# Kernel tuning notes

Measured on AMD Instinct MI355X. Metric: run time of the kernel, lower is better.

Reference implementation:

```python
import jax, jax.numpy as jnp
import numpy as np

BS = 128
HW = 128
REG = 0.1


def setup_inputs() -> dict:
    key = jax.random.key(0)
    k1, k2 = jax.random.split(key)
    x1 = jax.random.normal(k1, (BS, 1, HW, HW), dtype=jnp.float32)
    x2 = jax.random.normal(k2, (BS, 1, HW, HW), dtype=jnp.float32)
    return {"x1": x1, "x2": x2}


def _calc_psd(x):
    # x: [2*bs, H, W]
    dft = jnp.fft.fft2(x)
    avgpsd = jnp.mean((dft * jnp.conj(dft)).real, axis=0)  # [H, W]
    return jnp.mean(jnp.log(avgpsd)) - jnp.log(jnp.mean(avgpsd))


def reference(x1, x2):
    a = x1[:, 0]  # [bs, H, W] (squeeze channel)
    b = x2[:, 0]
    # pairwise Frobenius distances: Dist[i, j] = ||x1[i] - x2[j]||_F
    diff = a[:, None, :, :] - b[None, :, :, :]          # [bs, bs, H, W]
    Dist = jnp.sqrt(jnp.sum(diff * diff, axis=(-2, -1)))  # [bs, bs]
    bs = Dist.shape[0]
    # CrossEntropyLoss(Dist, arange(bs)) = mean_i(logsumexp(Dist[i]) - Dist[i, i])
    log_probs = jax.nn.log_softmax(Dist, axis=-1)
    ce = -jnp.mean(jnp.diagonal(log_probs))
    # PSD regularizer on cat(x1, x2)
    x = jnp.concatenate([a, b], axis=0)  # [2*bs, H, W]
    r = _calc_psd(x)
    return ce - REG * r
```

## Files before the change

kernel.cpp:

```cpp
#include <hip/hip_runtime.h>
#include <math.h>


#define WS_N     0
#define WS_G     256
#define WS_NP    16640
#define WS_GP    20736
#define WS_P     4215040
#define WS_PS    6344960
#define WS_PL    6345025

#define PI_F 3.14159265358979323846f

__global__ __launch_bounds__(256) void ocl_gram(const float* __restrict__ A_,
                                                const float* __restrict__ B_,
                                                float* __restrict__ ws) {
    __shared__ float4 As[128 * 16];
    __shared__ float4 Bs[128 * 16];
    int ks = blockIdx.x;
    int k0q = ks * 16;
    int t = threadIdx.x;
    const float4* A = (const float4*)A_;
    const float4* B = (const float4*)B_;

    {
        int qi = t & 15, r0 = t >> 4;
        #pragma unroll
        for (int p = 0; p < 8; ++p) {
            int r = r0 + 16 * p;
            int sq = qi ^ ((r >> 3) & 7);
            As[r * 16 + sq] = A[(size_t)r * 4096 + k0q + qi];
            Bs[r * 16 + sq] = B[(size_t)r * 4096 + k0q + qi];
        }
    }
    __syncthreads();

    int ty = t >> 4, tx = t & 15;
    float acc[8][8];
    #pragma unroll
    for (int r = 0; r < 8; ++r)
        #pragma unroll
        for (int c = 0; c < 8; ++c) acc[r][c] = 0.0f;

    for (int qk = 0; qk < 16; ++qk) {
        int sa = qk ^ (ty & 7);
        int sb = qk ^ (tx & 7);
        float4 a4[8], b4[8];
        #pragma unroll
        for (int r = 0; r < 8; ++r) a4[r] = As[(ty * 8 + r) * 16 + sa];
        #pragma unroll
        for (int c = 0; c < 8; ++c) b4[c] = Bs[(tx * 8 + c) * 16 + sb];
        #pragma unroll
        for (int r = 0; r < 8; ++r)
            #pragma unroll
            for (int c = 0; c < 8; ++c) {
                float4 a = a4[r], b = b4[c];
                acc[r][c] = fmaf(a.x, b.x, fmaf(a.y, b.y,
                            fmaf(a.z, b.z, fmaf(a.w, b.w, acc[r][c]))));
            }
    }

    float4* Gq = (float4*)(ws + WS_GP + (size_t)ks * 16384);
    #pragma unroll
    for (int r = 0; r < 8; ++r)
        #pragma unroll
        for (int cc = 0; cc < 2; ++cc)
            Gq[(ty * 8 + r) * 32 + tx * 2 + cc] =
                make_float4(acc[r][cc * 4 + 0], acc[r][cc * 4 + 1],
                            acc[r][cc * 4 + 2], acc[r][cc * 4 + 3]);
}

__device__ __forceinline__ void fft128_reg(float& s0r, float& s0i,
                                           float& s1r, float& s1i,
                                           float cA, float sA,
                                           const float* wr, const float* wi,
                                           int lane) {
    float er = s0r + s1r, ei = s0i + s1i;
    float dr = s0r - s1r, di = s0i - s1i;
    float orr = dr * cA - di * sA;
    float oii = dr * sA + di * cA;
    #pragma unroll
    for (int st = 0; st < 6; ++st) {
        int m = 32 >> st;
        bool up = (lane & m) == 0;
        float tr = __shfl_xor(er, m), ti = __shfl_xor(ei, m);
        float ar = tr - er, ai = ti - ei;
        float e2r = up ? (er + tr) : (ar * wr[st] - ai * wi[st]);
        float e2i = up ? (ei + ti) : (ar * wi[st] + ai * wr[st]);
        tr = __shfl_xor(orr, m); ti = __shfl_xor(oii, m);
        float br_ = tr - orr, bi_ = ti - oii;
        float o2r = up ? (orr + tr) : (br_ * wr[st] - bi_ * wi[st]);
        float o2i = up ? (oii + ti) : (br_ * wi[st] + bi_ * wr[st]);
        er = e2r; ei = e2i; orr = o2r; oii = o2i;
    }
    s0r = er; s0i = ei; s1r = orr; s1i = oii;
}

__global__ __launch_bounds__(1024) void ocl_fft_psd(const float* __restrict__ x1,
                                                    const float* __restrict__ x2,
                                                    float* __restrict__ ws) {
    __shared__ float zre[64 * 128];
    __shared__ float zim[64 * 128];
    int t = threadIdx.x, lane = t & 63, wave = t >> 6;
    int img = blockIdx.x;
    float* P = ws + WS_P + (size_t)img * 8320;
    const float* src = (img < 128) ? (x1 + (size_t)img * 16384)
                                   : (x2 + (size_t)(img - 128) * 16384);

    float cA, sA, wr[6], wi[6];
    {
        float th = -PI_F * (float)lane / 64.0f;
        sA = __sinf(th); cA = __cosf(th);
        #pragma unroll
        for (int st = 0; st < 6; ++st) {
            int m = 32 >> st;
            float a = -PI_F * (float)(lane & (m - 1)) / (float)m;
            wi[st] = __sinf(a); wr[st] = __cosf(a);
        }
    }
    int rb = (int)(__brev((unsigned)lane) >> 26);

    float nrm = 0.0f;
    #pragma unroll
    for (int pi = 0; pi < 4; ++pi) {
        int p = wave * 4 + pi;
        const float* r0 = src + p * 256 + lane;
        float s0r = r0[0],   s1r = r0[64];
        float s0i = r0[128], s1i = r0[192];
        nrm += s0r * s0r + s1r * s1r + s0i * s0i + s1i * s1i;
        fft128_reg(s0r, s0i, s1r, s1i, cA, sA, wr, wi, lane);
        int f0 = (2 * rb + p) & 127;
        int f1 = (2 * rb + 1 + p) & 127;
        zre[p * 128 + f0] = s0r; zim[p * 128 + f0] = s0i;
        zre[p * 128 + f1] = s1r; zim[p * 128 + f1] = s1i;
    }
    for (int off = 32; off >= 1; off >>= 1) nrm += __shfl_xor(nrm, off);
    if (lane == 0) ws[WS_NP + img * 16 + wave] = nrm;
    __syncthreads();

    int p0 = (lane >> 1), p1 = 32 + (lane >> 1);
    int par = lane & 1;
    for (int k = wave; k < 65; k += 16) {
        float v0r, v0i, v1r, v1i;
        if (k == 0 || k == 64) {
            int c0 = (k + p0) & 127, c1 = (k + p1) & 127;
            float Z0r = zre[p0 * 128 + c0], Z0i = zim[p0 * 128 + c0];
            float Z1r = zre[p1 * 128 + c1], Z1i = zim[p1 * 128 + c1];
            v0r = par ? Z0i : Z0r; v0i = 0.0f;
            v1r = par ? Z1i : Z1r; v1i = 0.0f;
        } else {
            int kn = 128 - k;
            int ck = (k + p0) & 127, cn = (kn + p0) & 127;
            float Zkr = zre[p0 * 128 + ck], Zki = zim[p0 * 128 + ck];
            float Znr = zre[p0 * 128 + cn], Zni = zim[p0 * 128 + cn];
            float e0r = 0.5f * (Zkr + Znr), e0i = 0.5f * (Zki - Zni);
            float q0r = 0.5f * (Zki + Zni), q0i = 0.5f * (Znr - Zkr);
            v0r = par ? q0r : e0r; v0i = par ? q0i : e0i;
            ck = (k + p1) & 127; cn = (kn + p1) & 127;
            Zkr = zre[p1 * 128 + ck]; Zki = zim[p1 * 128 + ck];
            Znr = zre[p1 * 128 + cn]; Zni = zim[p1 * 128 + cn];
            float e1r = 0.5f * (Zkr + Znr), e1i = 0.5f * (Zki - Zni);
            float q1r = 0.5f * (Zki + Zni), q1i = 0.5f * (Znr - Zkr);
            v1r = par ? q1r : e1r; v1i = par ? q1i : e1i;
        }
        fft128_reg(v0r, v0i, v1r, v1i, cA, sA, wr, wi, lane);
        P[k * 128 + lane]      = v0r * v0r + v0i * v0i;
        P[k * 128 + 64 + lane] = v1r * v1r + v1i * v1i;
    }
}

__global__ __launch_bounds__(256) void ocl_reduce(float* __restrict__ ws) {
    int bid = blockIdx.x, t = threadIdx.x;
    __shared__ float4 sh4[256];
    if (bid < 256) {
        int g = bid;
        const float4* Gp4 = (const float4*)(ws + WS_GP);
        int qi = t & 15, sg = t >> 4;
        float4 acc = make_float4(0.f, 0.f, 0.f, 0.f);
        #pragma unroll 4
        for (int it = 0; it < 16; ++it) {
            int sl = sg * 16 + it;
            float4 v = Gp4[(size_t)sl * 4096 + g * 16 + qi];
            acc.x += v.x; acc.y += v.y; acc.z += v.z; acc.w += v.w;
        }
        sh4[t] = acc;
        __syncthreads();
        if (t < 16) {
            float4 s = sh4[t];
            #pragma unroll
            for (int sg2 = 1; sg2 < 16; ++sg2) {
                float4 v = sh4[sg2 * 16 + t];
                s.x += v.x; s.y += v.y; s.z += v.z; s.w += v.w;
            }
            ((float4*)(ws + WS_G))[g * 16 + t] = s;
        }
    } else if (bid < 321) {
        int k = bid - 256;
        const float4* P4 = (const float4*)(ws + WS_P);
        int u4 = t & 31, ig = t >> 5;
        float4 acc = make_float4(0.f, 0.f, 0.f, 0.f);
        #pragma unroll 4
        for (int it = 0; it < 32; ++it) {
            int im = ig * 32 + it;
            float4 v = P4[(size_t)im * 2080 + k * 32 + u4];
            acc.x += v.x; acc.y += v.y; acc.z += v.z; acc.w += v.w;
        }
        sh4[t] = acc;
        __syncthreads();
        float sS = 0.0f, sL = 0.0f;
        if (t < 32) {
            float4 s = sh4[t];
            #pragma unroll
            for (int ig2 = 1; ig2 < 8; ++ig2) {
                float4 v = sh4[ig2 * 32 + t];
                s.x += v.x; s.y += v.y; s.z += v.z; s.w += v.w;
            }
            float w = (k == 0 || k == 64) ? 1.0f : 2.0f;
            sS = w * (s.x + s.y + s.z + s.w);
            sL = w * (logf(s.x) + logf(s.y) + logf(s.z) + logf(s.w));
        }
        #pragma unroll
        for (int off = 16; off >= 1; off >>= 1) {
            sS += __shfl_xor(sS, off);
            sL += __shfl_xor(sL, off);
        }
        if (t == 0) {
            ws[WS_PS + k] = sS;
            ws[WS_PL + k] = sL;
        }
    } else {
        const float* NP = ws + WS_NP + t * 16;
        float s = 0.0f;
        #pragma unroll
        for (int w = 0; w < 16; ++w) s += NP[w];
        ws[WS_N + t] = s;
    }
}

__global__ __launch_bounds__(1024) void ocl_tail(const float* __restrict__ ws,
                                                 float* __restrict__ out) {
    int t = threadIdx.x, lane = t & 63, wave = t >> 6;
    const float* na = ws + WS_N;
    const float* nb = ws + WS_N + 128;
    const float* G  = ws + WS_G;

    float rowacc = 0.0f;
    #pragma unroll
    for (int ri = 0; ri < 8; ++ri) {
        int i = wave * 8 + ri;
        int j0 = lane, j1 = 64 + lane;
        size_t b = (size_t)i * 128;
        float d0 = sqrtf(fmaxf(na[i] + nb[j0] - 2.0f * G[b + j0], 0.0f));
        float d1 = sqrtf(fmaxf(na[i] + nb[j1] - 2.0f * G[b + j1], 0.0f));
        float mx = fmaxf(d0, d1);
        for (int off = 32; off >= 1; off >>= 1) mx = fmaxf(mx, __shfl_xor(mx, off));
        float sm = expf(d0 - mx) + expf(d1 - mx);
        for (int off = 32; off >= 1; off >>= 1) sm += __shfl_xor(sm, off);
        float dii = (i < 64) ? __shfl(d0, i) : __shfl(d1, i - 64);
        rowacc += mx + logf(sm) - dii;
    }

    float sS = 0.0f, sL = 0.0f;
    if (t < 65) { sS = ws[WS_PS + t]; sL = ws[WS_PL + t]; }
    for (int off = 32; off >= 1; off >>= 1) {
        sS += __shfl_xor(sS, off);
        sL += __shfl_xor(sL, off);
    }
    __shared__ float aS[16], aL[16], aR[16];
    if (lane == 0) { aS[wave] = sS; aL[wave] = sL; aR[wave] = rowacc; }
    __syncthreads();
    if (t == 0) {
        float S_ = 0.0f, L_ = 0.0f, R_ = 0.0f;
        #pragma unroll
        for (int w = 0; w < 16; ++w) { S_ += aS[w]; L_ += aL[w]; R_ += aR[w]; }
        float ce = R_ / 128.0f;
        float r  = L_ / 16384.0f - logf(S_ / 16384.0f);
        out[0] = ce - 0.1f * r;
    }
}

extern "C" void kernel_launch(void* const* d_in, const int* in_sizes, int n_in,
                              void* d_out, int out_size, void* d_ws, size_t ws_size,
                              hipStream_t stream) {
    (void)in_sizes; (void)n_in; (void)out_size; (void)ws_size;
    const float* x1 = (const float*)d_in[0];
    const float* x2 = (const float*)d_in[1];
    float* ws  = (float*)d_ws;
    float* out = (float*)d_out;

    hipLaunchKernelGGL(ocl_gram,    dim3(256), dim3(256),  0, stream, x1, x2, ws);
    hipLaunchKernelGGL(ocl_fft_psd, dim3(256), dim3(1024), 0, stream, x1, x2, ws);
    hipLaunchKernelGGL(ocl_reduce,  dim3(322), dim3(256),  0, stream, ws);
    hipLaunchKernelGGL(ocl_tail,    dim3(1),   dim3(1024), 0, stream, ws, out);
}
```

Baseline: 106.1 us.

## Merge gram and FFT kernels into one launch and fold tail into reduce

Result: slower. 147.2 us (+38.7%).

```diff
diff --git a/kernel.cpp b/kernel.cpp
--- a/kernel.cpp
+++ b/kernel.cpp
@@ -9,66 +9,9 @@
 #define WS_P     4215040
 #define WS_PS    6344960
 #define WS_PL    6345025
+#define WS_CNT   6345090
 
 #define PI_F 3.14159265358979323846f
-
-__global__ __launch_bounds__(256) void ocl_gram(const float* __restrict__ A_,
-                                                const float* __restrict__ B_,
-                                                float* __restrict__ ws) {
-    __shared__ float4 As[128 * 16];
-    __shared__ float4 Bs[128 * 16];
-    int ks = blockIdx.x;
-    int k0q = ks * 16;
-    int t = threadIdx.x;
-    const float4* A = (const float4*)A_;
-    const float4* B = (const float4*)B_;
-
-    {
-        int qi = t & 15, r0 = t >> 4;
-        #pragma unroll
-        for (int p = 0; p < 8; ++p) {
-            int r = r0 + 16 * p;
-            int sq = qi ^ ((r >> 3) & 7);
-            As[r * 16 + sq] = A[(size_t)r * 4096 + k0q + qi];
-            Bs[r * 16 + sq] = B[(size_t)r * 4096 + k0q + qi];
-        }
-    }
-    __syncthreads();
-
-    int ty = t >> 4, tx = t & 15;
-    float acc[8][8];
-    #pragma unroll
-    for (int r = 0; r < 8; ++r)
-        #pragma unroll
-        for (int c = 0; c < 8; ++c) acc[r][c] = 0.0f;
-
-    for (int qk = 0; qk < 16; ++qk) {
-        int sa = qk ^ (ty & 7);
-        int sb = qk ^ (tx & 7);
-        float4 a4[8], b4[8];
-        #pragma unroll
-        for (int r = 0; r < 8; ++r) a4[r] = As[(ty * 8 + r) * 16 + sa];
-        #pragma unroll
-        for (int c = 0; c < 8; ++c) b4[c] = Bs[(tx * 8 + c) * 16 + sb];
-        #pragma unroll
-        for (int r = 0; r < 8; ++r)
-            #pragma unroll
-            for (int c = 0; c < 8; ++c) {
-                float4 a = a4[r], b = b4[c];
-                acc[r][c] = fmaf(a.x, b.x, fmaf(a.y, b.y,
-                            fmaf(a.z, b.z, fmaf(a.w, b.w, acc[r][c]))));
-            }
-    }
-
-    float4* Gq = (float4*)(ws + WS_GP + (size_t)ks * 16384);
-    #pragma unroll
-    for (int r = 0; r < 8; ++r)
-        #pragma unroll
-        for (int cc = 0; cc < 2; ++cc)
-            Gq[(ty * 8 + r) * 32 + tx * 2 + cc] =
-                make_float4(acc[r][cc * 4 + 0], acc[r][cc * 4 + 1],
-                            acc[r][cc * 4 + 2], acc[r][cc * 4 + 3]);
-}
 
 __device__ __forceinline__ void fft128_reg(float& s0r, float& s0i,
                                            float& s1r, float& s1i,
@@ -96,82 +39,147 @@
     s0r = er; s0i = ei; s1r = orr; s1i = oii;
 }
 
-__global__ __launch_bounds__(1024) void ocl_fft_psd(const float* __restrict__ x1,
-                                                    const float* __restrict__ x2,
-                                                    float* __restrict__ ws) {
-    __shared__ float zre[64 * 128];
-    __shared__ float zim[64 * 128];
-    int t = threadIdx.x, lane = t & 63, wave = t >> 6;
-    int img = blockIdx.x;
-    float* P = ws + WS_P + (size_t)img * 8320;
-    const float* src = (img < 128) ? (x1 + (size_t)img * 16384)
-                                   : (x2 + (size_t)(img - 128) * 16384);
-
-    float cA, sA, wr[6], wi[6];
-    {
-        float th = -PI_F * (float)lane / 64.0f;
-        sA = __sinf(th); cA = __cosf(th);
-        #pragma unroll
-        for (int st = 0; st < 6; ++st) {
-            int m = 32 >> st;
-            float a = -PI_F * (float)(lane & (m - 1)) / (float)m;
-            wi[st] = __sinf(a); wr[st] = __cosf(a);
-        }
-    }
-    int rb = (int)(__brev((unsigned)lane) >> 26);
-
-    float nrm = 0.0f;
-    #pragma unroll
-    for (int pi = 0; pi < 4; ++pi) {
-        int p = wave * 4 + pi;
-        const float* r0 = src + p * 256 + lane;
-        float s0r = r0[0],   s1r = r0[64];
-        float s0i = r0[128], s1i = r0[192];
-        nrm += s0r * s0r + s1r * s1r + s0i * s0i + s1i * s1i;
-        fft128_reg(s0r, s0i, s1r, s1i, cA, sA, wr, wi, lane);
-        int f0 = (2 * rb + p) & 127;
-        int f1 = (2 * rb + 1 + p) & 127;
-        zre[p * 128 + f0] = s0r; zim[p * 128 + f0] = s0i;
-        zre[p * 128 + f1] = s1r; zim[p * 128 + f1] = s1i;
-    }
-    for (int off = 32; off >= 1; off >>= 1) nrm += __shfl_xor(nrm, off);
-    if (lane == 0) ws[WS_NP + img * 16 + wave] = nrm;
-    __syncthreads();
-
-    int p0 = (lane >> 1), p1 = 32 + (lane >> 1);
-    int par = lane & 1;
-    for (int k = wave; k < 65; k += 16) {
-        float v0r, v0i, v1r, v1i;
-        if (k == 0 || k == 64) {
-            int c0 = (k + p0) & 127, c1 = (k + p1) & 127;
-            float Z0r = zre[p0 * 128 + c0], Z0i = zim[p0 * 128 + c0];
-            float Z1r = zre[p1 * 128 + c1], Z1i = zim[p1 * 128 + c1];
-            v0r = par ? Z0i : Z0r; v0i = 0.0f;
-            v1r = par ? Z1i : Z1r; v1i = 0.0f;
-        } else {
-            int kn = 128 - k;
-            int ck = (k + p0) & 127, cn = (kn + p0) & 127;
-            float Zkr = zre[p0 * 128 + ck], Zki = zim[p0 * 128 + ck];
-            float Znr = zre[p0 * 128 + cn], Zni = zim[p0 * 128 + cn];
-            float e0r = 0.5f * (Zkr + Znr), e0i = 0.5f * (Zki - Zni);
-            float q0r = 0.5f * (Zki + Zni), q0i = 0.5f * (Znr - Zkr);
-            v0r = par ? q0r : e0r; v0i = par ? q0i : e0i;
-            ck = (k + p1) & 127; cn = (kn + p1) & 127;
-            Zkr = zre[p1 * 128 + ck]; Zki = zim[p1 * 128 + ck];
-            Znr = zre[p1 * 128 + cn]; Zni = zim[p1 * 128 + cn];
-            float e1r = 0.5f * (Zkr + Znr), e1i = 0.5f * (Zki - Zni);
-            float q1r = 0.5f * (Zki + Zni), q1i = 0.5f * (Znr - Zkr);
-            v1r = par ? q1r : e1r; v1i = par ? q1i : e1i;
-        }
-        fft128_reg(v0r, v0i, v1r, v1i, cA, sA, wr, wi, lane);
-        P[k * 128 + lane]      = v0r * v0r + v0i * v0i;
-        P[k * 128 + 64 + lane] = v1r * v1r + v1i * v1i;
+__global__ __launch_bounds__(512) void ocl_main(const float* __restrict__ x1,
+                                                const float* __restrict__ x2,
+                                                float* __restrict__ ws) {
+    __shared__ float4 smem4[4096];
+    int t = threadIdx.x;
+    int bid = blockIdx.x;
+
+    if (bid < 256) {
+        if (bid == 0 && t == 0) *((int*)(ws + WS_CNT)) = 0;
+        float4* As = smem4;
+        float4* Bs = smem4 + 2048;
+        int ks = bid, k0q = ks * 16;
+        const float4* A = (const float4*)x1;
+        const float4* B = (const float4*)x2;
+        {
+            int qi = t & 15, r0 = t >> 4;
+            #pragma unroll
+            for (int p = 0; p < 4; ++p) {
+                int r = r0 + 32 * p;
+                int sq = qi ^ ((r >> 3) & 7);
+                As[r * 16 + sq] = A[(size_t)r * 4096 + k0q + qi];
+                Bs[r * 16 + sq] = B[(size_t)r * 4096 + k0q + qi];
+            }
+        }
+        __syncthreads();
+
+        int ty = t >> 4, tx = t & 15;
+        float acc[4][8];
+        #pragma unroll
+        for (int r = 0; r < 4; ++r)
+            #pragma unroll
+            for (int c = 0; c < 8; ++c) acc[r][c] = 0.0f;
+
+        for (int qk = 0; qk < 16; ++qk) {
+            float4 a4[4], b4[8];
+            #pragma unroll
+            for (int r = 0; r < 4; ++r) {
+                int rr = ty * 4 + r;
+                a4[r] = As[rr * 16 + (qk ^ ((rr >> 3) & 7))];
+            }
+            #pragma unroll
+            for (int c = 0; c < 8; ++c) {
+                int rc = tx * 8 + c;
+                b4[c] = Bs[rc * 16 + (qk ^ ((rc >> 3) & 7))];
+            }
+            #pragma unroll
+            for (int r = 0; r < 4; ++r)
+                #pragma unroll
+                for (int c = 0; c < 8; ++c) {
+                    float4 a = a4[r], b = b4[c];
+                    acc[r][c] = fmaf(a.x, b.x, fmaf(a.y, b.y,
+                                fmaf(a.z, b.z, fmaf(a.w, b.w, acc[r][c]))));
+                }
+        }
+
+        float4* Gq = (float4*)(ws + WS_GP + (size_t)ks * 16384);
+        #pragma unroll
+        for (int r = 0; r < 4; ++r)
+            #pragma unroll
+            for (int cc = 0; cc < 2; ++cc)
+                Gq[(ty * 4 + r) * 32 + tx * 2 + cc] =
+                    make_float4(acc[r][cc * 4 + 0], acc[r][cc * 4 + 1],
+                                acc[r][cc * 4 + 2], acc[r][cc * 4 + 3]);
+    } else {
+        float* zre = (float*)smem4;
+        float* zim = zre + 8192;
+        int lane = t & 63, wave = t >> 6;
+        int img = bid - 256;
+        float* P = ws + WS_P + (size_t)img * 8320;
+        const float* src = (img < 128) ? (x1 + (size_t)img * 16384)
+                                       : (x2 + (size_t)(img - 128) * 16384);
+
+        float cA, sA, wr[6], wi[6];
+        {
+            float th = -PI_F * (float)lane / 64.0f;
+            sA = __sinf(th); cA = __cosf(th);
+            #pragma unroll
+            for (int st = 0; st < 6; ++st) {
+                int m = 32 >> st;
+                float a = -PI_F * (float)(lane & (m - 1)) / (float)m;
+                wi[st] = __sinf(a); wr[st] = __cosf(a);
+            }
+        }
+        int rb = (int)(__brev((unsigned)lane) >> 26);
+
+        float nrm = 0.0f;
+        #pragma unroll
+        for (int pi = 0; pi < 8; ++pi) {
+            int p = wave * 8 + pi;
+            const float* r0 = src + p * 256 + lane;
+            float s0r = r0[0],   s1r = r0[64];
+            float s0i = r0[128], s1i = r0[192];
+            nrm += s0r * s0r + s1r * s1r + s0i * s0i + s1i * s1i;
+            fft128_reg(s0r, s0i, s1r, s1i, cA, sA, wr, wi, lane);
+            int f0 = (2 * rb + p) & 127;
+            int f1 = (2 * rb + 1 + p) & 127;
+            zre[p * 128 + f0] = s0r; zim[p * 128 + f0] = s0i;
+            zre[p * 128 + f1] = s1r; zim[p * 128 + f1] = s1i;
+        }
+        for (int off = 32; off >= 1; off >>= 1) nrm += __shfl_xor(nrm, off);
+        if (lane == 0) ws[WS_NP + img * 8 + wave] = nrm;
+        __syncthreads();
+
+        int p0 = (lane >> 1), p1 = 32 + (lane >> 1);
+        int par = lane & 1;
+        for (int k = wave; k < 65; k += 8) {
+            float v0r, v0i, v1r, v1i;
+            if (k == 0 || k == 64) {
+                int c0 = (k + p0) & 127, c1 = (k + p1) & 127;
+                float Z0r = zre[p0 * 128 + c0], Z0i = zim[p0 * 128 + c0];
+                float Z1r = zre[p1 * 128 + c1], Z1i = zim[p1 * 128 + c1];
+                v0r = par ? Z0i : Z0r; v0i = 0.0f;
+                v1r = par ? Z1i : Z1r; v1i = 0.0f;
+            } else {
+                int kn = 128 - k;
+                int ck = (k + p0) & 127, cn = (kn + p0) & 127;
+                float Zkr = zre[p0 * 128 + ck], Zki = zim[p0 * 128 + ck];
+                float Znr = zre[p0 * 128 + cn], Zni = zim[p0 * 128 + cn];
+                float e0r = 0.5f * (Zkr + Znr), e0i = 0.5f * (Zki - Zni);
+                float q0r = 0.5f * (Zki + Zni), q0i = 0.5f * (Znr - Zkr);
+                v0r = par ? q0r : e0r; v0i = par ? q0i : e0i;
+                ck = (k + p1) & 127; cn = (kn + p1) & 127;
+                Zkr = zre[p1 * 128 + ck]; Zki = zim[p1 * 128 + ck];
+                Znr = zre[p1 * 128 + cn]; Zni = zim[p1 * 128 + cn];
+                float e1r = 0.5f * (Zkr + Znr), e1i = 0.5f * (Zki - Zni);
+                float q1r = 0.5f * (Zki + Zni), q1i = 0.5f * (Znr - Zkr);
+                v1r = par ? q1r : e1r; v1i = par ? q1i : e1i;
+            }
+            fft128_reg(v0r, v0i, v1r, v1i, cA, sA, wr, wi, lane);
+            P[k * 128 + lane]      = v0r * v0r + v0i * v0i;
+            P[k * 128 + 64 + lane] = v1r * v1r + v1i * v1i;
+        }
     }
 }
 
-__global__ __launch_bounds__(256) void ocl_reduce(float* __restrict__ ws) {
+__global__ __launch_bounds__(256) void ocl_finish(float* __restrict__ ws,
+                                                  float* __restrict__ out) {
     int bid = blockIdx.x, t = threadIdx.x;
+    int lane = t & 63, wave = t >> 6;
     __shared__ float4 sh4[256];
+
     if (bid < 256) {
         int g = bid;
         const float4* Gp4 = (const float4*)(ws + WS_GP);
@@ -229,25 +237,29 @@
             ws[WS_PL + k] = sL;
         }
     } else {
-        const float* NP = ws + WS_NP + t * 16;
+        const float* NP = ws + WS_NP + t * 8;
         float s = 0.0f;
         #pragma unroll
-        for (int w = 0; w < 16; ++w) s += NP[w];
+        for (int w = 0; w < 8; ++w) s += NP[w];
         ws[WS_N + t] = s;
     }
-}
-
-__global__ __launch_bounds__(1024) void ocl_tail(const float* __restrict__ ws,
-                                                 float* __restrict__ out) {
-    int t = threadIdx.x, lane = t & 63, wave = t >> 6;
+
+    __threadfence();
+    __shared__ int lastflag;
+    if (t == 0) {
+        int old = atomicAdd((int*)(ws + WS_CNT), 1);
+        lastflag = (old == 321) ? 1 : 0;
+    }
+    __syncthreads();
+    if (!lastflag) return;
+    __threadfence();
+
     const float* na = ws + WS_N;
     const float* nb = ws + WS_N + 128;
     const float* G  = ws + WS_G;
-
     float rowacc = 0.0f;
-    #pragma unroll
-    for (int ri = 0; ri < 8; ++ri) {
-        int i = wave * 8 + ri;
+    for (int ri = 0; ri < 32; ++ri) {
+        int i = wave * 32 + ri;
         int j0 = lane, j1 = 64 + lane;
         size_t b = (size_t)i * 128;
         float d0 = sqrtf(fmaxf(na[i] + nb[j0] - 2.0f * G[b + j0], 0.0f));
@@ -266,13 +278,13 @@
         sS += __shfl_xor(sS, off);
         sL += __shfl_xor(sL, off);
     }
-    __shared__ float aS[16], aL[16], aR[16];
+    __shared__ float aS[4], aL[4], aR[4];
     if (lane == 0) { aS[wave] = sS; aL[wave] = sL; aR[wave] = rowacc; }
     __syncthreads();
     if (t == 0) {
-        float S_ = 0.0f, L_ = 0.0f, R_ = 0.0f;
-        #pragma unroll
-        for (int w = 0; w < 16; ++w) { S_ += aS[w]; L_ += aL[w]; R_ += aR[w]; }
+        float S_ = aS[0] + aS[1] + aS[2] + aS[3];
+        float L_ = aL[0] + aL[1] + aL[2] + aL[3];
+        float R_ = aR[0] + aR[1] + aR[2] + aR[3];
         float ce = R_ / 128.0f;
         float r  = L_ / 16384.0f - logf(S_ / 16384.0f);
         out[0] = ce - 0.1f * r;
@@ -288,8 +300,6 @@
     float* ws  = (float*)d_ws;
     float* out = (float*)d_out;
 
-    hipLaunchKernelGGL(ocl_gram,    dim3(256), dim3(256),  0, stream, x1, x2, ws);
-    hipLaunchKernelGGL(ocl_fft_psd, dim3(256), dim3(1024), 0, stream, x1, x2, ws);
-    hipLaunchKernelGGL(ocl_reduce,  dim3(322), dim3(256),  0, stream, ws);
-    hipLaunchKernelGGL(ocl_tail,    dim3(1),   dim3(1024), 0, stream, ws, out);
+    hipLaunchKernelGGL(ocl_main,   dim3(512), dim3(512), 0, stream, x1, x2, ws);
+    hipLaunchKernelGGL(ocl_finish, dim3(322), dim3(256), 0, stream, ws, out);
 }
```
